# Kernel optimization log

Measured on AMD Instinct MI355X. Metric: run time of the kernel, lower is better.

Reference implementation:

```python
import jax, jax.numpy as jnp
import numpy as np
from jax import lax

B, T, D_IN = 512, 256, 64
N_NEURONS, D_STATE, D_OUT = 2048, 64, 10


def setup_inputs() -> dict:
    key = jax.random.key(0)
    k_seq, k_enc, k_bias, k_gain, k_sd, k_d = jax.random.split(key, 6)
    enc = jax.random.normal(k_enc, (N_NEURONS, D_IN + D_STATE), dtype=jnp.float32)
    # hypersphere strategy: unit-norm encoder rows
    enc = enc / jnp.linalg.norm(enc, axis=-1, keepdims=True)
    return {
        "seq": jax.random.normal(k_seq, (B, T, D_IN), dtype=jnp.float32),
        "encoders": enc,
        "bias": jax.random.normal(k_bias, (N_NEURONS,), dtype=jnp.float32),
        "gain": jax.random.uniform(k_gain, (N_NEURONS,), dtype=jnp.float32),
        "state_decoders": jax.random.normal(k_sd, (N_NEURONS, D_STATE), dtype=jnp.float32) * 0.02,
        "decoders": jax.random.normal(k_d, (N_NEURONS, D_OUT), dtype=jnp.float32) * 0.02,
    }


def reference(seq, encoders, bias, gain, state_decoders, decoders):
    # seq: (B, T, d_in). Recurrent decode-then-re-encode loop over T.
    b = seq.shape[0]
    d_state = state_decoders.shape[1]
    n = encoders.shape[0]

    def step(carry, u_t):
        s, _ = carry  # s: (B, d_state)
        x_aug = jnp.concatenate([u_t, s], axis=-1)  # (B, d_in + d_state)
        a = jnp.abs(gain * (x_aug @ encoders.T) + bias)  # (B, n_neurons), activation='abs'
        s_new = a @ state_decoders  # (B, d_state)
        return (s_new, a), None

    s0 = jnp.zeros((b, d_state), dtype=seq.dtype)
    a0 = jnp.zeros((b, n), dtype=seq.dtype)
    (_, a_final), _ = lax.scan(step, (s0, a0), jnp.swapaxes(seq, 0, 1))
    return a_final @ decoders  # (B, d_out)
```

## Files before the change

kernel.cpp:

```cpp
#include <hip/hip_runtime.h>
#include <math.h>

#define B_    512
#define T_    256
#define DIN   64
#define DS    64
#define KK    128
#define NN    2048
#define DOUT  10

#define NT      512
#define BT      8
#define NTILES  (NN / NT)
#define BTILES  (B_ / BT)
#define THREADS 512
#define NWG     (NTILES * BTILES)

#define PSQ_ELEMS  ((size_t)BTILES * NTILES * BT * DS)
#define PS_FLOATS  (4 * PSQ_ELEMS)
#define ETSW_OFF   PS_FLOATS
#define ETSW_F16   ((size_t)KK * NN)
#define SDSW_OFF   (ETSW_OFF + ETSW_F16 / 2)
#define SDSW_F16   ((size_t)NN * DS)

typedef _Float16 half8 __attribute__((ext_vector_type(8)));
typedef float    f32x4 __attribute__((ext_vector_type(4)));

__global__ __launch_bounds__(256) void pre_kernel(const float* __restrict__ enc,
                                                  const float* __restrict__ sd,
                                                  float* __restrict__ ws,
                                                  float* __restrict__ out) {
    size_t i = (size_t)blockIdx.x * blockDim.x + threadIdx.x;
    size_t stride = (size_t)gridDim.x * blockDim.x;
    unsigned long long* psq = (unsigned long long*)ws;
    for (size_t x = i; x < 2 * PSQ_ELEMS; x += stride) psq[x] = 0ull;
    _Float16* EtSw = (_Float16*)(ws + ETSW_OFF);
    for (size_t x = i; x < (size_t)KK * NN; x += stride) {
        const int j     = (int)(x & 7);
        const int lane  = (int)((x >> 3) & 63);
        const int ktile = (int)((x >> 9) & 3);
        const int ntile = (int)((x >> 11) & 3);
        const int w     = (int)((x >> 13) & 7);
        const int nt    = (int)(x >> 16);
        const int n = nt * 512 + w * 64 + ntile * 16 + (lane & 15);
        const int k = ktile * 32 + ((lane >> 4) << 3) + j;
        EtSw[x] = (_Float16)enc[(size_t)n * KK + k];
    }
    _Float16* SdSw = (_Float16*)(ws + SDSW_OFF);
    for (size_t x = i; x < (size_t)NN * DS; x += stride) {
        const int j     = (int)(x & 7);
        const int lane  = (int)((x >> 3) & 63);
        const int ktile = (int)((x >> 9) & 15);
        const int cg    = (int)((x >> 13) & 3);
        const int nt    = (int)(x >> 15);
        const int n = nt * 512 + ktile * 32 + ((lane >> 4) << 3) + j;
        const int c = cg * 16 + (lane & 15);
        SdSw[x] = (_Float16)sd[(size_t)n * DS + c];
    }
    for (size_t x = i; x < (size_t)B_ * DOUT; x += stride) out[x] = 0.0f;
}

__global__ __launch_bounds__(THREADS, 1) void persist_kernel(
    const float* __restrict__ seq,
    const _Float16* __restrict__ EtSw,
    const _Float16* __restrict__ SdSw,
    const float* __restrict__ bias,
    const float* __restrict__ gain,
    const float* __restrict__ dec,
    unsigned long long* __restrict__ psq,
    float* __restrict__ out)
{
    __shared__ _Float16 xh[16][136];
    __shared__ _Float16 Ash[16][520];

    const int tid = threadIdx.x;
    const int nt = blockIdx.x & (NTILES - 1);
    const int bt = blockIdx.x >> 2;
    const int n0 = nt * NT;
    const int b0 = bt * BT;

    const int w = tid >> 6;
    const int l = tid & 63;
    const int rs = tid >> 6;
    const int cs = tid & 63;
    const int m16 = l & 15;
    const int q8  = (l >> 4) << 3;

    const _Float16* EtW = EtSw + ((size_t)(nt * 8 + w) << 13);
    const _Float16* SdW = SdSw + ((size_t)(nt * 4 + (w & 3)) << 13);

    half8 etf[4][4];
    #pragma unroll
    for (int n4 = 0; n4 < 4; ++n4)
        #pragma unroll
        for (int kt = 0; kt < 4; ++kt)
            etf[n4][kt] = *(const half8*)&EtW[(n4 << 11) + (kt << 9) + (size_t)l * 8];
    half8 sdf[16];
    #pragma unroll
    for (int kt = 0; kt < 16; ++kt)
        sdf[kt] = *(const half8*)&SdW[(kt << 9) + (size_t)l * 8];

    float gv[4], bv[4];
    #pragma unroll
    for (int n4 = 0; n4 < 4; ++n4) {
        gv[n4] = gain[n0 + w * 64 + n4 * 16 + m16];
        bv[n4] = bias[n0 + w * 64 + n4 * 16 + m16];
    }

    const size_t fan_base = ((size_t)bt * NTILES) * BT * DS + (size_t)rs * DS + cs;

    {
        unsigned int* xz = (unsigned int*)&xh[0][0];
        for (int i2 = tid; i2 < 16 * 136 / 2; i2 += THREADS) xz[i2] = 0u;
    }
    __syncthreads();

    float4 u0a = {0.f,0.f,0.f,0.f}, u0b = {0.f,0.f,0.f,0.f};
    float4 u1a = {0.f,0.f,0.f,0.f}, u1b = {0.f,0.f,0.f,0.f};
    if (m16 < 8) {
        const float* up = &seq[((size_t)(b0 + m16) * T_ + 0) * DIN];
        u0a = *(const float4*)&up[q8];
        u0b = *(const float4*)&up[q8 + 4];
        u1a = *(const float4*)&up[32 + q8];
        u1b = *(const float4*)&up[32 + q8 + 4];
    }

    for (int t = 0; t < T_; ++t) {
        const unsigned long long* pb =
            psq + (size_t)((t - 1) & 1) * PSQ_ELEMS + fan_base;
        unsigned long long v0 = 0, v1 = 0, v2 = 0, v3 = 0;
        if (t > 0) {
            v0 = __hip_atomic_load(pb + 0 * (BT * DS), __ATOMIC_RELAXED, __HIP_MEMORY_SCOPE_AGENT);
            v1 = __hip_atomic_load(pb + 1 * (BT * DS), __ATOMIC_RELAXED, __HIP_MEMORY_SCOPE_AGENT);
            v2 = __hip_atomic_load(pb + 2 * (BT * DS), __ATOMIC_RELAXED, __HIP_MEMORY_SCOPE_AGENT);
            v3 = __hip_atomic_load(pb + 3 * (BT * DS), __ATOMIC_RELAXED, __HIP_MEMORY_SCOPE_AGENT);
        }

        half8 af0, af1;
        af0[0] = (_Float16)u0a.x; af0[1] = (_Float16)u0a.y;
        af0[2] = (_Float16)u0a.z; af0[3] = (_Float16)u0a.w;
        af0[4] = (_Float16)u0b.x; af0[5] = (_Float16)u0b.y;
        af0[6] = (_Float16)u0b.z; af0[7] = (_Float16)u0b.w;
        af1[0] = (_Float16)u1a.x; af1[1] = (_Float16)u1a.y;
        af1[2] = (_Float16)u1a.z; af1[3] = (_Float16)u1a.w;
        af1[4] = (_Float16)u1b.x; af1[5] = (_Float16)u1b.y;
        af1[6] = (_Float16)u1b.z; af1[7] = (_Float16)u1b.w;

        if (m16 < 8 && t + 1 < T_) {
            const float* up = &seq[((size_t)(b0 + m16) * T_ + (t + 1)) * DIN];
            u0a = *(const float4*)&up[q8];
            u0b = *(const float4*)&up[q8 + 4];
            u1a = *(const float4*)&up[32 + q8];
            u1b = *(const float4*)&up[32 + q8 + 4];
        }

        f32x4 acc[4];
        #pragma unroll
        for (int n4 = 0; n4 < 4; ++n4) acc[n4] = (f32x4){0.f, 0.f, 0.f, 0.f};
        #pragma unroll
        for (int n4 = 0; n4 < 4; ++n4) {
            acc[n4] = __builtin_amdgcn_mfma_f32_16x16x32_f16(af0, etf[n4][0], acc[n4], 0, 0, 0);
            acc[n4] = __builtin_amdgcn_mfma_f32_16x16x32_f16(af1, etf[n4][1], acc[n4], 0, 0, 0);
        }

        if (t > 0) {
            const unsigned utag = (unsigned)t;
            for (;;) {
                if ((unsigned)(v0 >> 32) == utag && (unsigned)(v1 >> 32) == utag &&
                    (unsigned)(v2 >> 32) == utag && (unsigned)(v3 >> 32) == utag)
                    break;
                v0 = __hip_atomic_load(pb + 0 * (BT * DS), __ATOMIC_RELAXED, __HIP_MEMORY_SCOPE_AGENT);
                v1 = __hip_atomic_load(pb + 1 * (BT * DS), __ATOMIC_RELAXED, __HIP_MEMORY_SCOPE_AGENT);
                v2 = __hip_atomic_load(pb + 2 * (BT * DS), __ATOMIC_RELAXED, __HIP_MEMORY_SCOPE_AGENT);
                v3 = __hip_atomic_load(pb + 3 * (BT * DS), __ATOMIC_RELAXED, __HIP_MEMORY_SCOPE_AGENT);
            }
            const float ssum = __uint_as_float((unsigned)v0) + __uint_as_float((unsigned)v1)
                             + __uint_as_float((unsigned)v2) + __uint_as_float((unsigned)v3);
            xh[rs][DIN + cs] = (_Float16)ssum;
        } else {
            xh[rs][DIN + cs] = (_Float16)0.f;
        }
        __syncthreads();

        {
            const half8 af2 = *(const half8*)&xh[m16][64 + q8];
            const half8 af3 = *(const half8*)&xh[m16][96 + q8];
            #pragma unroll
            for (int n4 = 0; n4 < 4; ++n4) {
                acc[n4] = __builtin_amdgcn_mfma_f32_16x16x32_f16(af2, etf[n4][2], acc[n4], 0, 0, 0);
                acc[n4] = __builtin_amdgcn_mfma_f32_16x16x32_f16(af3, etf[n4][3], acc[n4], 0, 0, 0);
            }
        }

        if (l < 32) {
            const int rq = (l >> 4) << 2;
            #pragma unroll
            for (int n4 = 0; n4 < 4; ++n4) {
                const int n = w * 64 + n4 * 16 + m16;
                Ash[rq + 0][n] = (_Float16)fabsf(gv[n4] * acc[n4][0] + bv[n4]);
                Ash[rq + 1][n] = (_Float16)fabsf(gv[n4] * acc[n4][1] + bv[n4]);
                Ash[rq + 2][n] = (_Float16)fabsf(gv[n4] * acc[n4][2] + bv[n4]);
                Ash[rq + 3][n] = (_Float16)fabsf(gv[n4] * acc[n4][3] + bv[n4]);
            }
        }
        __syncthreads();

        if (t == T_ - 1) {
            for (int idx = tid; idx < BT * DOUT; idx += THREADS) {
                const int r = idx / DOUT;
                const int d = idx % DOUT;
                float o = 0.f;
                #pragma unroll 8
                for (int n = 0; n < NT; ++n)
                    o += (float)Ash[r][n] * dec[(size_t)(n0 + n) * DOUT + d];
                atomicAdd(&out[(size_t)(b0 + r) * DOUT + d], o);
            }
            return;
        }

        if (w < 4) {
            f32x4 d0 = (f32x4){0.f, 0.f, 0.f, 0.f};
            f32x4 d1 = (f32x4){0.f, 0.f, 0.f, 0.f};
            #pragma unroll
            for (int kt = 0; kt < 16; kt += 2) {
                const half8 a0 = *(const half8*)&Ash[m16][kt * 32 + q8];
                d0 = __builtin_amdgcn_mfma_f32_16x16x32_f16(a0, sdf[kt], d0, 0, 0, 0);
                const half8 a1 = *(const half8*)&Ash[m16][(kt + 1) * 32 + q8];
                d1 = __builtin_amdgcn_mfma_f32_16x16x32_f16(a1, sdf[kt + 1], d1, 0, 0, 0);
            }
            d0[0] += d1[0]; d0[1] += d1[1]; d0[2] += d1[2]; d0[3] += d1[3];
            if (l < 32) {
                const int rq = (l >> 4) << 2;
                unsigned long long* pw = psq + (size_t)(t & 1) * PSQ_ELEMS
                    + (((size_t)bt * NTILES + nt) * BT) * DS + 16 * w + m16;
                const unsigned long long tg = (unsigned long long)(unsigned)(t + 1) << 32;
                #pragma unroll
                for (int r = 0; r < 4; ++r) {
                    __hip_atomic_store(pw + (size_t)(rq + r) * DS,
                                       tg | (unsigned long long)__float_as_uint(d0[r]),
                                       __ATOMIC_RELAXED, __HIP_MEMORY_SCOPE_AGENT);
                }
            }
        }
    }
}

extern "C" void kernel_launch(void* const* d_in, const int* in_sizes, int n_in,
                              void* d_out, int out_size, void* d_ws, size_t ws_size,
                              hipStream_t stream) {
    const float* seq  = (const float*)d_in[0];
    const float* enc  = (const float*)d_in[1];
    const float* bias = (const float*)d_in[2];
    const float* gain = (const float*)d_in[3];
    const float* sd   = (const float*)d_in[4];
    const float* dec  = (const float*)d_in[5];
    float* out = (float*)d_out;
    float* ws  = (float*)d_ws;

    pre_kernel<<<dim3(1024), dim3(256), 0, stream>>>(enc, sd, ws, out);

    unsigned long long* psq = (unsigned long long*)ws;
    const _Float16* EtSw = (const _Float16*)(ws + ETSW_OFF);
    const _Float16* SdSw = (const _Float16*)(ws + SDSW_OFF);

    persist_kernel<<<dim3(NWG), dim3(THREADS), 0, stream>>>(
        seq, EtSw, SdSw, bias, gain, dec, psq, out);
}
```

Baseline: 610.3 us.

## Add fast sc0-load flag path with atomic fallback and remap blocks across XCDs

Each partial state is now written twice: into a second buffer with plain sc0 stores, and into the original buffer with relaxed agent-scope atomic stores. Consumers poll the sc0 buffer first using inline-asm loads and wave-uniform checks, spinning up to a fixed iteration count before falling back to the atomic buffer. A block that has to fall back twice switches to atomic-only polling for the rest of the run. The block-to-tile mapping is also permuted so the four N-tiles of each batch tile likely land on the same XCD, which would let the sc0 (L2-coherent) path see peer writes quickly; the cost is extra store traffic and reliance on the hardware's block placement.

Measured after the change: 703.9 us. 1.15x slower.

```diff
diff --git a/kernel.cpp b/kernel.cpp
--- a/kernel.cpp
+++ b/kernel.cpp
@@ -17,8 +17,8 @@
 #define NWG     (NTILES * BTILES)
 
 #define PSQ_ELEMS  ((size_t)BTILES * NTILES * BT * DS)
-#define PS_FLOATS  (4 * PSQ_ELEMS)
-#define ETSW_OFF   PS_FLOATS
+#define PSQF_OFF   (4 * PSQ_ELEMS)
+#define ETSW_OFF   (8 * PSQ_ELEMS)
 #define ETSW_F16   ((size_t)KK * NN)
 #define SDSW_OFF   (ETSW_OFF + ETSW_F16 / 2)
 #define SDSW_F16   ((size_t)NN * DS)
@@ -33,7 +33,7 @@
     size_t i = (size_t)blockIdx.x * blockDim.x + threadIdx.x;
     size_t stride = (size_t)gridDim.x * blockDim.x;
     unsigned long long* psq = (unsigned long long*)ws;
-    for (size_t x = i; x < 2 * PSQ_ELEMS; x += stride) psq[x] = 0ull;
+    for (size_t x = i; x < 4 * PSQ_ELEMS; x += stride) psq[x] = 0ull;
     _Float16* EtSw = (_Float16*)(ws + ETSW_OFF);
     for (size_t x = i; x < (size_t)KK * NN; x += stride) {
         const int j     = (int)(x & 7);
@@ -67,15 +67,18 @@
     const float* __restrict__ bias,
     const float* __restrict__ gain,
     const float* __restrict__ dec,
-    unsigned long long* __restrict__ psq,
+    unsigned long long* __restrict__ psqA,
+    unsigned long long* __restrict__ psqF,
     float* __restrict__ out)
 {
     __shared__ _Float16 xh[16][136];
     __shared__ _Float16 Ash[16][520];
 
     const int tid = threadIdx.x;
-    const int nt = blockIdx.x & (NTILES - 1);
-    const int bt = blockIdx.x >> 2;
+    const int r8 = blockIdx.x & 7;
+    const int s  = blockIdx.x >> 3;
+    const int nt = s & 3;
+    const int bt = r8 * 8 + (s >> 2);
     const int n0 = nt * NT;
     const int b0 = bt * BT;
 
@@ -125,15 +128,30 @@
         u1b = *(const float4*)&up[32 + q8 + 4];
     }
 
+    int fastfails = 0;
+    int slowmode  = 0;
+
     for (int t = 0; t < T_; ++t) {
-        const unsigned long long* pb =
-            psq + (size_t)((t - 1) & 1) * PSQ_ELEMS + fan_base;
+        const size_t par = (size_t)((t - 1) & 1);
+        const unsigned long long* pbF = psqF + par * PSQ_ELEMS + fan_base;
+        const unsigned long long* pbA = psqA + par * PSQ_ELEMS + fan_base;
         unsigned long long v0 = 0, v1 = 0, v2 = 0, v3 = 0;
         if (t > 0) {
-            v0 = __hip_atomic_load(pb + 0 * (BT * DS), __ATOMIC_RELAXED, __HIP_MEMORY_SCOPE_AGENT);
-            v1 = __hip_atomic_load(pb + 1 * (BT * DS), __ATOMIC_RELAXED, __HIP_MEMORY_SCOPE_AGENT);
-            v2 = __hip_atomic_load(pb + 2 * (BT * DS), __ATOMIC_RELAXED, __HIP_MEMORY_SCOPE_AGENT);
-            v3 = __hip_atomic_load(pb + 3 * (BT * DS), __ATOMIC_RELAXED, __HIP_MEMORY_SCOPE_AGENT);
+            if (slowmode == 0) {
+                asm volatile("global_load_dwordx2 %0, %4, off sc0\n\t"
+                             "global_load_dwordx2 %1, %5, off sc0\n\t"
+                             "global_load_dwordx2 %2, %6, off sc0\n\t"
+                             "global_load_dwordx2 %3, %7, off sc0"
+                             : "=&v"(v0), "=&v"(v1), "=&v"(v2), "=&v"(v3)
+                             : "v"(pbF + 0 * (BT * DS)), "v"(pbF + 1 * (BT * DS)),
+                               "v"(pbF + 2 * (BT * DS)), "v"(pbF + 3 * (BT * DS))
+                             : "memory");
+            } else {
+                v0 = __hip_atomic_load(pbA + 0 * (BT * DS), __ATOMIC_RELAXED, __HIP_MEMORY_SCOPE_AGENT);
+                v1 = __hip_atomic_load(pbA + 1 * (BT * DS), __ATOMIC_RELAXED, __HIP_MEMORY_SCOPE_AGENT);
+                v2 = __hip_atomic_load(pbA + 2 * (BT * DS), __ATOMIC_RELAXED, __HIP_MEMORY_SCOPE_AGENT);
+                v3 = __hip_atomic_load(pbA + 3 * (BT * DS), __ATOMIC_RELAXED, __HIP_MEMORY_SCOPE_AGENT);
+            }
         }
 
         half8 af0, af1;
@@ -165,14 +183,64 @@
 
         if (t > 0) {
             const unsigned utag = (unsigned)t;
-            for (;;) {
-                if ((unsigned)(v0 >> 32) == utag && (unsigned)(v1 >> 32) == utag &&
-                    (unsigned)(v2 >> 32) == utag && (unsigned)(v3 >> 32) == utag)
-                    break;
-                v0 = __hip_atomic_load(pb + 0 * (BT * DS), __ATOMIC_RELAXED, __HIP_MEMORY_SCOPE_AGENT);
-                v1 = __hip_atomic_load(pb + 1 * (BT * DS), __ATOMIC_RELAXED, __HIP_MEMORY_SCOPE_AGENT);
-                v2 = __hip_atomic_load(pb + 2 * (BT * DS), __ATOMIC_RELAXED, __HIP_MEMORY_SCOPE_AGENT);
-                v3 = __hip_atomic_load(pb + 3 * (BT * DS), __ATOMIC_RELAXED, __HIP_MEMORY_SCOPE_AGENT);
+            if (slowmode == 0) {
+                asm volatile("s_waitcnt vmcnt(0)"
+                             : "+v"(v0), "+v"(v1), "+v"(v2), "+v"(v3) :: "memory");
+                __builtin_amdgcn_sched_barrier(0);
+                bool allf = ((unsigned)(v0 >> 32) == utag) & ((unsigned)(v1 >> 32) == utag)
+                          & ((unsigned)(v2 >> 32) == utag) & ((unsigned)(v3 >> 32) == utag);
+                if (!__all(allf)) {
+                    bool fb = false;
+                    int it = 0;
+                    while (!__all((unsigned)(v0 >> 32) == utag)) {
+                        if (++it > 24) { fb = true; break; }
+                        asm volatile("global_load_dwordx2 %0, %1, off sc0\n\t"
+                                     "s_waitcnt vmcnt(0)"
+                                     : "=v"(v0) : "v"(pbF + 0 * (BT * DS)) : "memory");
+                        __builtin_amdgcn_sched_barrier(0);
+                    }
+                    if (!fb) {
+                        it = 0;
+                        for (;;) {
+                            asm volatile("global_load_dwordx2 %0, %3, off sc0\n\t"
+                                         "global_load_dwordx2 %1, %4, off sc0\n\t"
+                                         "global_load_dwordx2 %2, %5, off sc0\n\t"
+                                         "s_waitcnt vmcnt(0)"
+                                         : "=&v"(v1), "=&v"(v2), "=&v"(v3)
+                                         : "v"(pbF + 1 * (BT * DS)),
+                                           "v"(pbF + 2 * (BT * DS)),
+                                           "v"(pbF + 3 * (BT * DS))
+                                         : "memory");
+                            __builtin_amdgcn_sched_barrier(0);
+                            if (__all(((unsigned)(v1 >> 32) == utag)
+                                    & ((unsigned)(v2 >> 32) == utag)
+                                    & ((unsigned)(v3 >> 32) == utag))) break;
+                            if (++it > 16) { fb = true; break; }
+                        }
+                    }
+                    if (fb) {
+                        for (;;) {
+                            v0 = __hip_atomic_load(pbA + 0 * (BT * DS), __ATOMIC_RELAXED, __HIP_MEMORY_SCOPE_AGENT);
+                            v1 = __hip_atomic_load(pbA + 1 * (BT * DS), __ATOMIC_RELAXED, __HIP_MEMORY_SCOPE_AGENT);
+                            v2 = __hip_atomic_load(pbA + 2 * (BT * DS), __ATOMIC_RELAXED, __HIP_MEMORY_SCOPE_AGENT);
+                            v3 = __hip_atomic_load(pbA + 3 * (BT * DS), __ATOMIC_RELAXED, __HIP_MEMORY_SCOPE_AGENT);
+                            if ((unsigned)(v0 >> 32) == utag && (unsigned)(v1 >> 32) == utag &&
+                                (unsigned)(v2 >> 32) == utag && (unsigned)(v3 >> 32) == utag)
+                                break;
+                        }
+                        if (++fastfails >= 2) slowmode = 1;
+                    }
+                }
+            } else {
+                for (;;) {
+                    if ((unsigned)(v0 >> 32) == utag && (unsigned)(v1 >> 32) == utag &&
+                        (unsigned)(v2 >> 32) == utag && (unsigned)(v3 >> 32) == utag)
+                        break;
+                    v0 = __hip_atomic_load(pbA + 0 * (BT * DS), __ATOMIC_RELAXED, __HIP_MEMORY_SCOPE_AGENT);
+                    v1 = __hip_atomic_load(pbA + 1 * (BT * DS), __ATOMIC_RELAXED, __HIP_MEMORY_SCOPE_AGENT);
+                    v2 = __hip_atomic_load(pbA + 2 * (BT * DS), __ATOMIC_RELAXED, __HIP_MEMORY_SCOPE_AGENT);
+                    v3 = __hip_atomic_load(pbA + 3 * (BT * DS), __ATOMIC_RELAXED, __HIP_MEMORY_SCOPE_AGENT);
+                }
             }
             const float ssum = __uint_as_float((unsigned)v0) + __uint_as_float((unsigned)v1)
                              + __uint_as_float((unsigned)v2) + __uint_as_float((unsigned)v3);
@@ -231,15 +299,24 @@
             d0[0] += d1[0]; d0[1] += d1[1]; d0[2] += d1[2]; d0[3] += d1[3];
             if (l < 32) {
                 const int rq = (l >> 4) << 2;
-                unsigned long long* pw = psq + (size_t)(t & 1) * PSQ_ELEMS
+                const size_t slot = (size_t)(t & 1) * PSQ_ELEMS
                     + (((size_t)bt * NTILES + nt) * BT) * DS + 16 * w + m16;
+                unsigned long long* pwF = psqF + slot;
+                unsigned long long* pwA = psqA + slot;
                 const unsigned long long tg = (unsigned long long)(unsigned)(t + 1) << 32;
+                unsigned long long vals[4];
                 #pragma unroll
-                for (int r = 0; r < 4; ++r) {
-                    __hip_atomic_store(pw + (size_t)(rq + r) * DS,
-                                       tg | (unsigned long long)__float_as_uint(d0[r]),
+                for (int r = 0; r < 4; ++r)
+                    vals[r] = tg | (unsigned long long)__float_as_uint(d0[r]);
+                #pragma unroll
+                for (int r = 0; r < 4; ++r)
+                    asm volatile("global_store_dwordx2 %0, %1, off sc0"
+                                 :: "v"(pwF + (size_t)(rq + r) * DS), "v"(vals[r])
+                                 : "memory");
+                #pragma unroll
+                for (int r = 0; r < 4; ++r)
+                    __hip_atomic_store(pwA + (size_t)(rq + r) * DS, vals[r],
                                        __ATOMIC_RELAXED, __HIP_MEMORY_SCOPE_AGENT);
-                }
             }
         }
     }
@@ -259,10 +336,11 @@
 
     pre_kernel<<<dim3(1024), dim3(256), 0, stream>>>(enc, sd, ws, out);
 
-    unsigned long long* psq = (unsigned long long*)ws;
+    unsigned long long* psqA = (unsigned long long*)ws;
+    unsigned long long* psqF = (unsigned long long*)(ws + PSQF_OFF);
     const _Float16* EtSw = (const _Float16*)(ws + ETSW_OFF);
     const _Float16* SdSw = (const _Float16*)(ws + SDSW_OFF);
 
     persist_kernel<<<dim3(NWG), dim3(THREADS), 0, stream>>>(
-        seq, EtSw, SdSw, bias, gain, dec, psq, out);
+        seq, EtSw, SdSw, bias, gain, dec, psqA, psqF, out);
 }
```
